# Optimization experiments

Hardware: AMD Instinct MI355X
Metric: run time of the kernel (lower is better)

## Reference

```python
import jax, jax.numpy as jnp
import numpy as np

NEG_BIG = -9e15  # matches torch's -9000000000000000.0 mask value


def _gat_layer(x, adj_mask, W, a):
    # x: [N, Fin], W: [Fin, Fout], a: [Fout]
    h = x @ W                                   # [N, Fout]
    d = jnp.abs(h[None, :, :] - h[:, None, :])  # [N, N, Fout] pairwise |h_j - h_i|
    e = jax.nn.relu(jnp.einsum('ijf,f->ij', d, a))
    e = jnp.where(adj_mask, e, NEG_BIG)
    att = jax.nn.softmax(e, axis=1)             # row softmax (dropout p=0, skipped)
    return jax.nn.relu(att @ h)


def setup_inputs() -> dict:
    key = jax.random.key(0)
    ks = jax.random.split(key, 10)
    N, F, H, C = 1024, 128, 128, 16

    def xavier(k, shape, gain=1.414):
        fan_in, fan_out = shape[0], shape[-1]
        bound = gain * np.sqrt(6.0 / (fan_in + fan_out))
        return jax.random.uniform(k, shape, jnp.float32, -bound, bound)

    feat = jax.random.normal(ks[0], (N, F), jnp.float32)
    adj = jax.random.randint(ks[1], (N, N), 0, 2, jnp.int32)
    return {
        'feat': feat,
        'adj': adj,
        'W1': xavier(ks[2], (F, H)), 'a1': xavier(ks[3], (H, 1)).squeeze(-1),
        'W2': xavier(ks[4], (H, H)), 'a2': xavier(ks[5], (H, 1)).squeeze(-1),
        'W3': xavier(ks[6], (H, H)), 'a3': xavier(ks[7], (H, 1)).squeeze(-1),
        'Wfc': xavier(ks[8], (H, C), gain=1.0),
        'bfc': jnp.zeros((C,), jnp.float32),
    }


def reference(feat, adj, W1, a1, W2, a2, W3, a3, Wfc, bfc):
    mask = adj > 0
    x = _gat_layer(feat, mask, W1, a1)
    x = _gat_layer(x, mask, W2, a2)
    x = _gat_layer(x, mask, W3, a3)
    # EdgeGCN (include_adj=False): pairwise abs-diff -> linear, output [N*N, C]
    N, H = x.shape
    diff = jnp.abs(x[None, :, :] - x[:, None, :]).reshape(N * N, H)
    return diff @ Wfc + bfc
```

## Files before the change

### kernel.cpp

```cpp
#include <hip/hip_runtime.h>
#include <math.h>

#define NEG_BIG -9.0e15f

typedef __attribute__((ext_vector_type(4))) float f32x4;
typedef __attribute__((ext_vector_type(8))) short bf16x8;

__global__ __launch_bounds__(128) void gemm_xw_t(const float* __restrict__ X,
                                                 const float* __restrict__ W,
                                                 float* __restrict__ HT) {
  __shared__ float xrow[128];
  const int i = blockIdx.x;
  const int o = threadIdx.x;
  xrow[o] = X[(size_t)i * 128 + o];
  __syncthreads();
  float acc = 0.f;
#pragma unroll 16
  for (int k = 0; k < 128; ++k) acc = fmaf(xrow[k], W[(size_t)k * 128 + o], acc);
  HT[(size_t)o * 1024 + i] = acc;
}

#define ABSFMA4(acc, hv, ha)                        \
  acc.x = fmaf(fabsf(hv.x - ha.x), ha.y, acc.x);    \
  acc.y = fmaf(fabsf(hv.y - ha.x), ha.y, acc.y);    \
  acc.z = fmaf(fabsf(hv.z - ha.x), ha.y, acc.z);    \
  acc.w = fmaf(fabsf(hv.w - ha.x), ha.y, acc.w);

#define DOT4(acc, hv, p) \
  acc = fmaf(hv.x, p.x, fmaf(hv.y, p.y, fmaf(hv.z, p.z, fmaf(hv.w, p.w, acc))));

__global__ __launch_bounds__(1024, 4) void gat_attn(const float* __restrict__ HT,
                                                    const int* __restrict__ adj,
                                                    const float* __restrict__ a,
                                                    float* __restrict__ Xout) {
  __shared__ float ep2[2][4][1024];
  __shared__ float e_s[4][1024];
  __shared__ float2 ha_s[4][128];
  __shared__ float redm[4][4];
  __shared__ float redsum[4][4];
  __shared__ float inv_s[4];

  const int t = threadIdx.x;
  const int i0 = blockIdx.x * 4;
  const float4* __restrict__ HT4 = reinterpret_cast<const float4*>(HT);

  if (t < 512) {
    const int pil = t >> 7;
    const int f = t & 127;
    ha_s[pil][f] = make_float2(HT[(size_t)f * 1024 + i0 + pil], a[f]);
  }
  __syncthreads();

  const int ih = t >> 9;
  const int fh = (t >> 8) & 1;
  const int jt = t & 255;
  const int il = t >> 8;
  const int j0 = (t & 255) * 4;

  float4 esum = {0.f, 0.f, 0.f, 0.f};
#pragma unroll
  for (int pass = 0; pass < 2; ++pass) {
    const int fb = pass * 64 + fh * 32;
    float4 aA = {0.f, 0.f, 0.f, 0.f};
    float4 aB = {0.f, 0.f, 0.f, 0.f};
#pragma unroll 4
    for (int ff = 0; ff < 32; ++ff) {
      const int f = fb + ff;
      const float4 hv = HT4[f * 256 + jt];
      const float2 hA = ha_s[ih * 2][f];
      const float2 hB = ha_s[ih * 2 + 1][f];
      ABSFMA4(aA, hv, hA);
      ABSFMA4(aB, hv, hB);
    }
    *reinterpret_cast<float4*>(&ep2[fh][ih * 2][jt * 4]) = aA;
    *reinterpret_cast<float4*>(&ep2[fh][ih * 2 + 1][jt * 4]) = aB;
    __syncthreads();
    {
      const float4 s0 = *reinterpret_cast<const float4*>(&ep2[0][il][j0]);
      const float4 s1 = *reinterpret_cast<const float4*>(&ep2[1][il][j0]);
      esum.x += s0.x + s1.x;
      esum.y += s0.y + s1.y;
      esum.z += s0.z + s1.z;
      esum.w += s0.w + s1.w;
    }
    __syncthreads();
  }

  float4 e;
  {
    const int4 ad = *reinterpret_cast<const int4*>(&adj[(size_t)(i0 + il) * 1024 + j0]);
    e.x = ad.x > 0 ? fmaxf(esum.x, 0.f) : NEG_BIG;
    e.y = ad.y > 0 ? fmaxf(esum.y, 0.f) : NEG_BIG;
    e.z = ad.z > 0 ? fmaxf(esum.z, 0.f) : NEG_BIG;
    e.w = ad.w > 0 ? fmaxf(esum.w, 0.f) : NEG_BIG;
  }

  const int wq = (t >> 6) & 3;
  float m = fmaxf(fmaxf(e.x, e.y), fmaxf(e.z, e.w));
#pragma unroll
  for (int off = 32; off > 0; off >>= 1) m = fmaxf(m, __shfl_xor(m, off));
  if ((t & 63) == 0) redm[il][wq] = m;
  __syncthreads();
  m = fmaxf(fmaxf(redm[il][0], redm[il][1]), fmaxf(redm[il][2], redm[il][3]));
  float4 p;
  p.x = __expf(e.x - m);
  p.y = __expf(e.y - m);
  p.z = __expf(e.z - m);
  p.w = __expf(e.w - m);
  *reinterpret_cast<float4*>(&e_s[il][j0]) = p;
  float s = p.x + p.y + p.z + p.w;
#pragma unroll
  for (int off = 32; off > 0; off >>= 1) s += __shfl_xor(s, off);
  if ((t & 63) == 0) redsum[il][wq] = s;
  __syncthreads();
  if (t < 4) {
    const float ss = redsum[t][0] + redsum[t][1] + redsum[t][2] + redsum[t][3];
    inv_s[t] = 1.f / ss;
  }
  __syncthreads();

  const int w = t >> 6;
  const int l = t & 63;
  const int f0 = w * 8;
  float acc[8][4];
#pragma unroll
  for (int ff = 0; ff < 8; ++ff)
#pragma unroll
    for (int r = 0; r < 4; ++r) acc[ff][r] = 0.f;

#pragma unroll
  for (int jb = 0; jb < 4; ++jb) {
    const int j4 = jb * 64 + l;
    const float4 p0 = *reinterpret_cast<const float4*>(&e_s[0][j4 * 4]);
    const float4 p1 = *reinterpret_cast<const float4*>(&e_s[1][j4 * 4]);
    const float4 p2 = *reinterpret_cast<const float4*>(&e_s[2][j4 * 4]);
    const float4 p3 = *reinterpret_cast<const float4*>(&e_s[3][j4 * 4]);
#pragma unroll
    for (int ff = 0; ff < 8; ++ff) {
      const float4 hv = HT4[(f0 + ff) * 256 + j4];
      DOT4(acc[ff][0], hv, p0);
      DOT4(acc[ff][1], hv, p1);
      DOT4(acc[ff][2], hv, p2);
      DOT4(acc[ff][3], hv, p3);
    }
  }

  float v[32];
#pragma unroll
  for (int ff = 0; ff < 8; ++ff)
#pragma unroll
    for (int r = 0; r < 4; ++r) v[ff * 4 + r] = acc[ff][r];

#pragma unroll
  for (int step = 0; step < 5; ++step) {
    const int s2 = 1 << step;
    const bool hi = (l & s2) != 0;
#pragma unroll
    for (int k = 0; k < (32 >> (step + 1)); ++k) {
      const float x = v[2 * k];
      const float y = v[2 * k + 1];
      float tt = hi ? x : y;
      tt = __shfl_xor(tt, s2);
      v[k] = (hi ? y : x) + tt;
    }
  }
  float r = v[0] + __shfl_xor(v[0], 32);

  if (l < 32) {
    const int oidx = l & 31;
    const int ff = oidx >> 2;
    const int orow = oidx & 3;
    const float o = fmaxf(r * inv_s[orow], 0.f);
    Xout[(size_t)(i0 + orow) * 128 + f0 + ff] = o;
  }
}

__global__ __launch_bounds__(256) void edge_fc_mfma(const float* __restrict__ X,
                                                    const float* __restrict__ Wfc,
                                                    const float* __restrict__ bfc,
                                                    float* __restrict__ out) {
  __shared__ float xi_s[32][132];
  __shared__ float xj_s[32][132];

  const int t = threadIdx.x;
  const int bid = blockIdx.x;
  int jb = (int)((sqrtf(8.0f * (float)bid + 1.0f) - 1.0f) * 0.5f);
  int ib = bid - jb * (jb + 1) / 2;
  if (ib > jb) { jb++; ib = bid - jb * (jb + 1) / 2; }
  if (ib < 0) { jb--; ib = bid - jb * (jb + 1) / 2; }

  {
    const int r = t >> 3;
    const int c0 = (t & 7) * 16;
    const float4* gi = reinterpret_cast<const float4*>(X + (size_t)(ib * 32 + r) * 128 + c0);
    const float4* gj = reinterpret_cast<const float4*>(X + (size_t)(jb * 32 + r) * 128 + c0);
#pragma unroll
    for (int k = 0; k < 4; ++k) {
      *reinterpret_cast<float4*>(&xi_s[r][c0 + k * 4]) = gi[k];
      *reinterpret_cast<float4*>(&xj_s[r][c0 + k * 4]) = gj[k];
    }
  }

  const int w = t >> 6;
  const int lane = t & 63;
  const int col = lane & 15;
  const int kg = lane >> 4;

  bf16x8 bhi[4], blo[4];
#pragma unroll
  for (int c = 0; c < 4; ++c) {
    bf16x8 bh, bl;
#pragma unroll
    for (int j = 0; j < 8; ++j) {
      const float wv = Wfc[(c * 32 + kg * 8 + j) * 16 + col];
      const unsigned u = __builtin_bit_cast(unsigned, wv);
      const unsigned h = u & 0xffff0000u;
      const float lof = wv - __builtin_bit_cast(float, h);
      bh[j] = (short)(h >> 16);
      bl[j] = (short)(__builtin_bit_cast(unsigned, lof) >> 16);
    }
    bhi[c] = bh;
    blo[c] = bl;
  }
  const float bb = bfc[col];

  __syncthreads();

  const int j0 = (w & 1) * 16;
  const int ih = w >> 1;
  float xjr[4][8];
#pragma unroll
  for (int c = 0; c < 4; ++c) {
    const float4 v0 = *reinterpret_cast<const float4*>(&xj_s[j0 + col][c * 32 + kg * 8]);
    const float4 v1 = *reinterpret_cast<const float4*>(&xj_s[j0 + col][c * 32 + kg * 8 + 4]);
    xjr[c][0] = v0.x; xjr[c][1] = v0.y; xjr[c][2] = v0.z; xjr[c][3] = v0.w;
    xjr[c][4] = v1.x; xjr[c][5] = v1.y; xjr[c][6] = v1.z; xjr[c][7] = v1.w;
  }

  const int gjbase = jb * 32 + j0 + kg * 4;
  const bool mirror = (ib != jb);

  for (int i = 0; i < 16; ++i) {
    const int li = ih * 16 + i;
    f32x4 acc = {bb, bb, bb, bb};
#pragma unroll
    for (int c = 0; c < 4; ++c) {
      const float4 v0 = *reinterpret_cast<const float4*>(&xi_s[li][c * 32 + kg * 8]);
      const float4 v1 = *reinterpret_cast<const float4*>(&xi_s[li][c * 32 + kg * 8 + 4]);
      float xiv[8];
      xiv[0] = v0.x; xiv[1] = v0.y; xiv[2] = v0.z; xiv[3] = v0.w;
      xiv[4] = v1.x; xiv[5] = v1.y; xiv[6] = v1.z; xiv[7] = v1.w;
      bf16x8 ah, al;
#pragma unroll
      for (int j = 0; j < 8; ++j) {
        const float d = fabsf(xjr[c][j] - xiv[j]);
        const unsigned u = __builtin_bit_cast(unsigned, d);
        const unsigned h = u & 0xffff0000u;
        const float lof = d - __builtin_bit_cast(float, h);
        ah[j] = (short)(h >> 16);
        al[j] = (short)(__builtin_bit_cast(unsigned, lof) >> 16);
      }
      acc = __builtin_amdgcn_mfma_f32_16x16x32_bf16(ah, bhi[c], acc, 0, 0, 0);
      acc = __builtin_amdgcn_mfma_f32_16x16x32_bf16(ah, blo[c], acc, 0, 0, 0);
      acc = __builtin_amdgcn_mfma_f32_16x16x32_bf16(al, bhi[c], acc, 0, 0, 0);
    }
    const int gi = ib * 32 + li;
#pragma unroll
    for (int r = 0; r < 4; ++r) {
      out[((size_t)gi * 1024 + gjbase + r) * 16 + col] = acc[r];
    }
    if (mirror) {
#pragma unroll
      for (int r = 0; r < 4; ++r) {
        out[((size_t)(gjbase + r) * 1024 + gi) * 16 + col] = acc[r];
      }
    }
  }
}

extern "C" void kernel_launch(void* const* d_in, const int* in_sizes, int n_in,
                              void* d_out, int out_size, void* d_ws, size_t ws_size,
                              hipStream_t stream) {
  const float* feat = (const float*)d_in[0];
  const int* adj = (const int*)d_in[1];
  const float* W1 = (const float*)d_in[2];
  const float* a1 = (const float*)d_in[3];
  const float* W2 = (const float*)d_in[4];
  const float* a2 = (const float*)d_in[5];
  const float* W3 = (const float*)d_in[6];
  const float* a3 = (const float*)d_in[7];
  const float* Wfc = (const float*)d_in[8];
  const float* bfc = (const float*)d_in[9];
  float* out = (float*)d_out;

  float* ht = (float*)d_ws;
  float* xA = ht + 131072;
  float* xB = xA + 131072;

  gemm_xw_t<<<1024, 128, 0, stream>>>(feat, W1, ht);
  gat_attn<<<256, 1024, 0, stream>>>(ht, adj, a1, xA);
  gemm_xw_t<<<1024, 128, 0, stream>>>(xA, W2, ht);
  gat_attn<<<256, 1024, 0, stream>>>(ht, adj, a2, xB);
  gemm_xw_t<<<1024, 128, 0, stream>>>(xB, W3, ht);
  gat_attn<<<256, 1024, 0, stream>>>(ht, adj, a3, xA);
  edge_fc_mfma<<<528, 256, 0, stream>>>(xA, Wfc, bfc, out);
}
```

Before: 107.9 us.

## Restructure GAT score loop and vectorize edge FC output stores

The attention kernel now gives each thread two full-feature j columns for two rows, which removes the split-feature partial sums, the shared-memory staging and two barriers. It reads the h_i values and the attention vector straight from global memory, and the final reciprocal of the softmax sum is folded into the output step. The edge FC kernel doubles its grid by splitting the i rows in half, loads the x_j values straight into registers, and packs the bf16 halves with a perm instruction. It also stages each MFMA result in shared memory so outputs go out as coalesced float4 stores. The aim is less synchronization, better store coalescing on the large output, and more parallelism, at the cost of repeated global loads of x_j and the per-f h_i row.

Result: slower. 123.1 us (+14.1%).

```diff
diff --git a/kernel.cpp b/kernel.cpp
--- a/kernel.cpp
+++ b/kernel.cpp
@@ -5,6 +5,7 @@
 
 typedef __attribute__((ext_vector_type(4))) float f32x4;
 typedef __attribute__((ext_vector_type(8))) short bf16x8;
+typedef __attribute__((ext_vector_type(4))) unsigned int u32x4;
 
 __global__ __launch_bounds__(128) void gemm_xw_t(const float* __restrict__ X,
                                                  const float* __restrict__ W,
@@ -20,12 +21,6 @@
   HT[(size_t)o * 1024 + i] = acc;
 }
 
-#define ABSFMA4(acc, hv, ha)                        \
-  acc.x = fmaf(fabsf(hv.x - ha.x), ha.y, acc.x);    \
-  acc.y = fmaf(fabsf(hv.y - ha.x), ha.y, acc.y);    \
-  acc.z = fmaf(fabsf(hv.z - ha.x), ha.y, acc.z);    \
-  acc.w = fmaf(fabsf(hv.w - ha.x), ha.y, acc.w);
-
 #define DOT4(acc, hv, p) \
   acc = fmaf(hv.x, p.x, fmaf(hv.y, p.y, fmaf(hv.z, p.z, fmaf(hv.w, p.w, acc))));
 
@@ -33,94 +28,77 @@
                                                     const int* __restrict__ adj,
                                                     const float* __restrict__ a,
                                                     float* __restrict__ Xout) {
-  __shared__ float ep2[2][4][1024];
   __shared__ float e_s[4][1024];
-  __shared__ float2 ha_s[4][128];
-  __shared__ float redm[4][4];
-  __shared__ float redsum[4][4];
-  __shared__ float inv_s[4];
+  __shared__ float redm[4][8];
+  __shared__ float redsum[4][8];
 
   const int t = threadIdx.x;
   const int i0 = blockIdx.x * 4;
+  const int ih = t >> 9;
+  const int jt = t & 511;
+  const int j0 = jt * 2;
+  const float2* __restrict__ HT2 = reinterpret_cast<const float2*>(HT);
   const float4* __restrict__ HT4 = reinterpret_cast<const float4*>(HT);
 
-  if (t < 512) {
-    const int pil = t >> 7;
-    const int f = t & 127;
-    ha_s[pil][f] = make_float2(HT[(size_t)f * 1024 + i0 + pil], a[f]);
-  }
-  __syncthreads();
-
-  const int ih = t >> 9;
-  const int fh = (t >> 8) & 1;
-  const int jt = t & 255;
-  const int il = t >> 8;
-  const int j0 = (t & 255) * 4;
-
-  float4 esum = {0.f, 0.f, 0.f, 0.f};
-#pragma unroll
-  for (int pass = 0; pass < 2; ++pass) {
-    const int fb = pass * 64 + fh * 32;
-    float4 aA = {0.f, 0.f, 0.f, 0.f};
-    float4 aB = {0.f, 0.f, 0.f, 0.f};
-#pragma unroll 4
-    for (int ff = 0; ff < 32; ++ff) {
-      const int f = fb + ff;
-      const float4 hv = HT4[f * 256 + jt];
-      const float2 hA = ha_s[ih * 2][f];
-      const float2 hB = ha_s[ih * 2 + 1][f];
-      ABSFMA4(aA, hv, hA);
-      ABSFMA4(aB, hv, hB);
-    }
-    *reinterpret_cast<float4*>(&ep2[fh][ih * 2][jt * 4]) = aA;
-    *reinterpret_cast<float4*>(&ep2[fh][ih * 2 + 1][jt * 4]) = aB;
-    __syncthreads();
-    {
-      const float4 s0 = *reinterpret_cast<const float4*>(&ep2[0][il][j0]);
-      const float4 s1 = *reinterpret_cast<const float4*>(&ep2[1][il][j0]);
-      esum.x += s0.x + s1.x;
-      esum.y += s0.y + s1.y;
-      esum.z += s0.z + s1.z;
-      esum.w += s0.w + s1.w;
-    }
-    __syncthreads();
-  }
-
-  float4 e;
-  {
-    const int4 ad = *reinterpret_cast<const int4*>(&adj[(size_t)(i0 + il) * 1024 + j0]);
-    e.x = ad.x > 0 ? fmaxf(esum.x, 0.f) : NEG_BIG;
-    e.y = ad.y > 0 ? fmaxf(esum.y, 0.f) : NEG_BIG;
-    e.z = ad.z > 0 ? fmaxf(esum.z, 0.f) : NEG_BIG;
-    e.w = ad.w > 0 ? fmaxf(esum.w, 0.f) : NEG_BIG;
-  }
-
-  const int wq = (t >> 6) & 3;
-  float m = fmaxf(fmaxf(e.x, e.y), fmaxf(e.z, e.w));
-#pragma unroll
-  for (int off = 32; off > 0; off >>= 1) m = fmaxf(m, __shfl_xor(m, off));
-  if ((t & 63) == 0) redm[il][wq] = m;
-  __syncthreads();
-  m = fmaxf(fmaxf(redm[il][0], redm[il][1]), fmaxf(redm[il][2], redm[il][3]));
-  float4 p;
-  p.x = __expf(e.x - m);
-  p.y = __expf(e.y - m);
-  p.z = __expf(e.z - m);
-  p.w = __expf(e.w - m);
-  *reinterpret_cast<float4*>(&e_s[il][j0]) = p;
-  float s = p.x + p.y + p.z + p.w;
-#pragma unroll
-  for (int off = 32; off > 0; off >>= 1) s += __shfl_xor(s, off);
-  if ((t & 63) == 0) redsum[il][wq] = s;
-  __syncthreads();
-  if (t < 4) {
-    const float ss = redsum[t][0] + redsum[t][1] + redsum[t][2] + redsum[t][3];
-    inv_s[t] = 1.f / ss;
-  }
-  __syncthreads();
+  float aA0 = 0.f, aA1 = 0.f, aB0 = 0.f, aB1 = 0.f;
+  for (int f4 = 0; f4 < 32; ++f4) {
+    const float4 a4 = *reinterpret_cast<const float4*>(a + f4 * 4);
+#pragma unroll
+    for (int k = 0; k < 4; ++k) {
+      const int f = f4 * 4 + k;
+      const float4 hr = *reinterpret_cast<const float4*>(HT + ((size_t)f << 10) + i0);
+      const float av = (k == 0) ? a4.x : (k == 1) ? a4.y : (k == 2) ? a4.z : a4.w;
+      const float hA = ih ? hr.z : hr.x;
+      const float hB = ih ? hr.w : hr.y;
+      const float2 hv = HT2[(f << 9) + jt];
+      aA0 = fmaf(fabsf(hv.x - hA), av, aA0);
+      aA1 = fmaf(fabsf(hv.y - hA), av, aA1);
+      aB0 = fmaf(fabsf(hv.x - hB), av, aB0);
+      aB1 = fmaf(fabsf(hv.y - hB), av, aB1);
+    }
+  }
+
+  const int rA = 2 * ih, rB = rA + 1;
+  const int2 adA = *reinterpret_cast<const int2*>(adj + (size_t)(i0 + rA) * 1024 + j0);
+  const int2 adB = *reinterpret_cast<const int2*>(adj + (size_t)(i0 + rB) * 1024 + j0);
+  const float eA0 = adA.x > 0 ? fmaxf(aA0, 0.f) : NEG_BIG;
+  const float eA1 = adA.y > 0 ? fmaxf(aA1, 0.f) : NEG_BIG;
+  const float eB0 = adB.x > 0 ? fmaxf(aB0, 0.f) : NEG_BIG;
+  const float eB1 = adB.y > 0 ? fmaxf(aB1, 0.f) : NEG_BIG;
 
   const int w = t >> 6;
   const int l = t & 63;
+  float mA = fmaxf(eA0, eA1), mB = fmaxf(eB0, eB1);
+#pragma unroll
+  for (int off = 32; off > 0; off >>= 1) {
+    mA = fmaxf(mA, __shfl_xor(mA, off));
+    mB = fmaxf(mB, __shfl_xor(mB, off));
+  }
+  if (l == 0) { redm[rA][w & 7] = mA; redm[rB][w & 7] = mB; }
+  __syncthreads();
+  {
+    const float4 m0 = *reinterpret_cast<const float4*>(&redm[rA][0]);
+    const float4 m1 = *reinterpret_cast<const float4*>(&redm[rA][4]);
+    mA = fmaxf(fmaxf(fmaxf(m0.x, m0.y), fmaxf(m0.z, m0.w)),
+               fmaxf(fmaxf(m1.x, m1.y), fmaxf(m1.z, m1.w)));
+    const float4 n0 = *reinterpret_cast<const float4*>(&redm[rB][0]);
+    const float4 n1 = *reinterpret_cast<const float4*>(&redm[rB][4]);
+    mB = fmaxf(fmaxf(fmaxf(n0.x, n0.y), fmaxf(n0.z, n0.w)),
+               fmaxf(fmaxf(n1.x, n1.y), fmaxf(n1.z, n1.w)));
+  }
+  const float pA0 = __expf(eA0 - mA), pA1 = __expf(eA1 - mA);
+  const float pB0 = __expf(eB0 - mB), pB1 = __expf(eB1 - mB);
+  *reinterpret_cast<float2*>(&e_s[rA][j0]) = make_float2(pA0, pA1);
+  *reinterpret_cast<float2*>(&e_s[rB][j0]) = make_float2(pB0, pB1);
+  float sA = pA0 + pA1, sB = pB0 + pB1;
+#pragma unroll
+  for (int off = 32; off > 0; off >>= 1) {
+    sA += __shfl_xor(sA, off);
+    sB += __shfl_xor(sB, off);
+  }
+  if (l == 0) { redsum[rA][w & 7] = sA; redsum[rB][w & 7] = sB; }
+  __syncthreads();
+
   const int f0 = w * 8;
   float acc[8][4];
 #pragma unroll
@@ -150,7 +128,6 @@
   for (int ff = 0; ff < 8; ++ff)
 #pragma unroll
     for (int r = 0; r < 4; ++r) v[ff * 4 + r] = acc[ff][r];
-
 #pragma unroll
   for (int step = 0; step < 5; ++step) {
     const int s2 = 1 << step;
@@ -164,14 +141,16 @@
       v[k] = (hi ? y : x) + tt;
     }
   }
-  float r = v[0] + __shfl_xor(v[0], 32);
+  const float r0 = v[0] + __shfl_xor(v[0], 32);
 
   if (l < 32) {
     const int oidx = l & 31;
     const int ff = oidx >> 2;
     const int orow = oidx & 3;
-    const float o = fmaxf(r * inv_s[orow], 0.f);
-    Xout[(size_t)(i0 + orow) * 128 + f0 + ff] = o;
+    const float4 s0 = *reinterpret_cast<const float4*>(&redsum[orow][0]);
+    const float4 s1 = *reinterpret_cast<const float4*>(&redsum[orow][4]);
+    const float inv = 1.f / (s0.x + s0.y + s0.z + s0.w + s1.x + s1.y + s1.z + s1.w);
+    Xout[(size_t)(i0 + orow) * 128 + f0 + ff] = fmaxf(r0 * inv, 0.f);
   }
 }
 
@@ -179,11 +158,12 @@
                                                     const float* __restrict__ Wfc,
                                                     const float* __restrict__ bfc,
                                                     float* __restrict__ out) {
-  __shared__ float xi_s[32][132];
-  __shared__ float xj_s[32][132];
+  __shared__ float xi_s[32][128];
+  __shared__ float ostage[4][256];
 
   const int t = threadIdx.x;
-  const int bid = blockIdx.x;
+  const int bid = blockIdx.x >> 1;
+  const int half = blockIdx.x & 1;
   int jb = (int)((sqrtf(8.0f * (float)bid + 1.0f) - 1.0f) * 0.5f);
   int ib = bid - jb * (jb + 1) / 2;
   if (ib > jb) { jb++; ib = bid - jb * (jb + 1) / 2; }
@@ -193,18 +173,13 @@
     const int r = t >> 3;
     const int c0 = (t & 7) * 16;
     const float4* gi = reinterpret_cast<const float4*>(X + (size_t)(ib * 32 + r) * 128 + c0);
-    const float4* gj = reinterpret_cast<const float4*>(X + (size_t)(jb * 32 + r) * 128 + c0);
-#pragma unroll
-    for (int k = 0; k < 4; ++k) {
-      *reinterpret_cast<float4*>(&xi_s[r][c0 + k * 4]) = gi[k];
-      *reinterpret_cast<float4*>(&xj_s[r][c0 + k * 4]) = gj[k];
-    }
-  }
-
-  const int w = t >> 6;
-  const int lane = t & 63;
-  const int col = lane & 15;
-  const int kg = lane >> 4;
+#pragma unroll
+    for (int k = 0; k < 4; ++k) *reinterpret_cast<float4*>(&xi_s[r][c0 + k * 4]) = gi[k];
+  }
+
+  const int w = t >> 6, lane = t & 63;
+  const int col = lane & 15, kg = lane >> 4;
+  const int ih = w >> 1, j0 = (w & 1) * 16;
 
   bf16x8 bhi[4], blo[4];
 #pragma unroll
@@ -224,57 +199,75 @@
   }
   const float bb = bfc[col];
 
+  unsigned xjr[4][8];
+#pragma unroll
+  for (int c = 0; c < 4; ++c) {
+    const float4 v0 = *reinterpret_cast<const float4*>(
+        X + (size_t)(jb * 32 + j0 + col) * 128 + c * 32 + kg * 8);
+    const float4 v1 = *reinterpret_cast<const float4*>(
+        X + (size_t)(jb * 32 + j0 + col) * 128 + c * 32 + kg * 8 + 4);
+    xjr[c][0] = __builtin_bit_cast(unsigned, v0.x);
+    xjr[c][1] = __builtin_bit_cast(unsigned, v0.y);
+    xjr[c][2] = __builtin_bit_cast(unsigned, v0.z);
+    xjr[c][3] = __builtin_bit_cast(unsigned, v0.w);
+    xjr[c][4] = __builtin_bit_cast(unsigned, v1.x);
+    xjr[c][5] = __builtin_bit_cast(unsigned, v1.y);
+    xjr[c][6] = __builtin_bit_cast(unsigned, v1.z);
+    xjr[c][7] = __builtin_bit_cast(unsigned, v1.w);
+  }
+
   __syncthreads();
 
-  const int j0 = (w & 1) * 16;
-  const int ih = w >> 1;
-  float xjr[4][8];
-#pragma unroll
-  for (int c = 0; c < 4; ++c) {
-    const float4 v0 = *reinterpret_cast<const float4*>(&xj_s[j0 + col][c * 32 + kg * 8]);
-    const float4 v1 = *reinterpret_cast<const float4*>(&xj_s[j0 + col][c * 32 + kg * 8 + 4]);
-    xjr[c][0] = v0.x; xjr[c][1] = v0.y; xjr[c][2] = v0.z; xjr[c][3] = v0.w;
-    xjr[c][4] = v1.x; xjr[c][5] = v1.y; xjr[c][6] = v1.z; xjr[c][7] = v1.w;
-  }
-
-  const int gjbase = jb * 32 + j0 + kg * 4;
   const bool mirror = (ib != jb);
-
-  for (int i = 0; i < 16; ++i) {
-    const int li = ih * 16 + i;
+  const int li_base = ih * 16 + half * 8;
+
+  for (int i = 0; i < 8; ++i) {
+    const int li = li_base + i;
+    const int gi = ib * 32 + li;
     f32x4 acc = {bb, bb, bb, bb};
 #pragma unroll
     for (int c = 0; c < 4; ++c) {
       const float4 v0 = *reinterpret_cast<const float4*>(&xi_s[li][c * 32 + kg * 8]);
       const float4 v1 = *reinterpret_cast<const float4*>(&xi_s[li][c * 32 + kg * 8 + 4]);
-      float xiv[8];
-      xiv[0] = v0.x; xiv[1] = v0.y; xiv[2] = v0.z; xiv[3] = v0.w;
-      xiv[4] = v1.x; xiv[5] = v1.y; xiv[6] = v1.z; xiv[7] = v1.w;
-      bf16x8 ah, al;
-#pragma unroll
-      for (int j = 0; j < 8; ++j) {
-        const float d = fabsf(xjr[c][j] - xiv[j]);
-        const unsigned u = __builtin_bit_cast(unsigned, d);
-        const unsigned h = u & 0xffff0000u;
-        const float lof = d - __builtin_bit_cast(float, h);
-        ah[j] = (short)(h >> 16);
-        al[j] = (short)(__builtin_bit_cast(unsigned, lof) >> 16);
+      unsigned xiv[8];
+      xiv[0] = __builtin_bit_cast(unsigned, v0.x);
+      xiv[1] = __builtin_bit_cast(unsigned, v0.y);
+      xiv[2] = __builtin_bit_cast(unsigned, v0.z);
+      xiv[3] = __builtin_bit_cast(unsigned, v0.w);
+      xiv[4] = __builtin_bit_cast(unsigned, v1.x);
+      xiv[5] = __builtin_bit_cast(unsigned, v1.y);
+      xiv[6] = __builtin_bit_cast(unsigned, v1.z);
+      xiv[7] = __builtin_bit_cast(unsigned, v1.w);
+      u32x4 ahv, alv;
+#pragma unroll
+      for (int q = 0; q < 4; ++q) {
+        const float d0 = __builtin_bit_cast(float, xjr[c][2 * q]) -
+                         __builtin_bit_cast(float, xiv[2 * q]);
+        const float d1 = __builtin_bit_cast(float, xjr[c][2 * q + 1]) -
+                         __builtin_bit_cast(float, xiv[2 * q + 1]);
+        const unsigned h0 = __builtin_bit_cast(unsigned, d0) & 0x7fff0000u;
+        const unsigned h1 = __builtin_bit_cast(unsigned, d1) & 0x7fff0000u;
+        const float lo0 = fabsf(d0) - __builtin_bit_cast(float, h0);
+        const float lo1 = fabsf(d1) - __builtin_bit_cast(float, h1);
+        ahv[q] = __builtin_amdgcn_perm(h1, h0, 0x07060302u);
+        alv[q] = __builtin_amdgcn_perm(__builtin_bit_cast(unsigned, lo1),
+                                       __builtin_bit_cast(unsigned, lo0), 0x07060302u);
       }
+      const bf16x8 ah = __builtin_bit_cast(bf16x8, ahv);
+      const bf16x8 al = __builtin_bit_cast(bf16x8, alv);
       acc = __builtin_amdgcn_mfma_f32_16x16x32_bf16(ah, bhi[c], acc, 0, 0, 0);
       acc = __builtin_amdgcn_mfma_f32_16x16x32_bf16(ah, blo[c], acc, 0, 0, 0);
       acc = __builtin_amdgcn_mfma_f32_16x16x32_bf16(al, bhi[c], acc, 0, 0, 0);
     }
-    const int gi = ib * 32 + li;
-#pragma unroll
-    for (int r = 0; r < 4; ++r) {
-      out[((size_t)gi * 1024 + gjbase + r) * 16 + col] = acc[r];
-    }
-    if (mirror) {
-#pragma unroll
-      for (int r = 0; r < 4; ++r) {
-        out[((size_t)(gjbase + r) * 1024 + gi) * 16 + col] = acc[r];
-      }
-    }
+#pragma unroll
+    for (int r = 0; r < 4; ++r) ostage[w][(kg * 4 + r) * 16 + col] = acc[r];
+    const float4 vv = *reinterpret_cast<const float4*>(&ostage[w][lane * 4]);
+    const int jl = lane >> 2;
+    const int c0 = (lane & 3) * 4;
+    const int gj = jb * 32 + j0 + jl;
+    *reinterpret_cast<float4*>(out + ((size_t)gi * 1024 + gj) * 16 + c0) = vv;
+    if (mirror)
+      *reinterpret_cast<float4*>(out + ((size_t)gj * 1024 + gi) * 16 + c0) = vv;
   }
 }
 
@@ -303,5 +296,5 @@
   gat_attn<<<256, 1024, 0, stream>>>(ht, adj, a2, xB);
   gemm_xw_t<<<1024, 128, 0, stream>>>(xB, W3, ht);
   gat_attn<<<256, 1024, 0, stream>>>(ht, adj, a3, xA);
-  edge_fc_mfma<<<528, 256, 0, stream>>>(xA, Wfc, bfc, out);
+  edge_fc_mfma<<<1056, 256, 0, stream>>>(xA, Wfc, bfc, out);
 }
```
